# Kernel optimization log

Measured on AMD Instinct MI355X. Metric: run time of the kernel, lower is better.

## Reference

```python
import jax, jax.numpy as jnp
import numpy as np

EPS = 1e-12
N_HEADS = 16


def _ln(x, g, b, eps=EPS):
    m = jnp.mean(x, axis=-1, keepdims=True)
    v = jnp.var(x, axis=-1, keepdims=True)
    return (x - m) * jax.lax.rsqrt(v + eps) * g + b


def setup_inputs() -> dict:
    key = jax.random.key(0)
    ks = jax.random.split(key, 8)
    B, S, D, I = 2, 2048, 1024, 4096
    s = 0.02
    f32 = jnp.float32
    return {
        "x": jax.random.normal(ks[0], (B, S, D), f32),
        "input_mask": jnp.zeros((B, 1, 1, S), f32),  # additive mask, 0 = no masking
        "norm_w": jnp.ones((D,), f32),
        "norm_b": jnp.zeros((D,), f32),
        "attn_qkvw": jax.random.normal(ks[1], (D, 3 * D), f32) * s,
        "attn_qkvb": jnp.zeros((3 * D,), f32),
        "attn_ow": jax.random.normal(ks[2], (D, D), f32) * s,
        "attn_ob": jnp.zeros((D,), f32),
        "attn_nw": jnp.ones((D,), f32),
        "attn_nb": jnp.zeros((D,), f32),
        "inter_w": jax.random.normal(ks[3], (D, I), f32) * s,
        "inter_b": jnp.zeros((I,), f32),
        "inter_w1": jax.random.normal(ks[4], (D, I), f32) * s,
        "output_w": jax.random.normal(ks[5], (I, D), f32) * s,
        "output_b": jnp.zeros((D,), f32),
    }


def reference(x, input_mask, norm_w, norm_b, attn_qkvw, attn_qkvb, attn_ow,
              attn_ob, attn_nw, attn_nb, inter_w, inter_b, inter_w1,
              output_w, output_b):
    B, S, D = x.shape
    hd = D // N_HEADS

    # --- fused qkv_gemm: pre-layernorm + QKV GEMM + bias ---
    ln1 = _ln(x, norm_w, norm_b)
    qkv = ln1 @ attn_qkvw + attn_qkvb            # [B,S,3D]
    q, k, v = jnp.split(qkv, 3, axis=-1)

    def to_heads(t):  # [B,S,D] -> [B,H,S,hd]
        return t.reshape(B, S, N_HEADS, hd).transpose(0, 2, 1, 3)

    q, k, v = to_heads(q), to_heads(k), to_heads(v)

    # --- softmax-context attention (scale_attention=True -> 1/sqrt(head_dim)) ---
    scores = jnp.einsum('bhqd,bhkd->bhqk', q, k) / jnp.sqrt(jnp.float32(hd))
    scores = scores + input_mask                 # additive mask [B,1,1,S]
    probs = jax.nn.softmax(scores, axis=-1)
    ctx = jnp.einsum('bhqk,bhkd->bhqd', probs, v)
    ctx = ctx.transpose(0, 2, 1, 3).reshape(B, S, D)

    attn_out = ctx @ attn_ow                     # vector_matmul (no bias)

    # --- fused mlp_gemm: bias+residual add, layernorm, GEMM+bias+gelu ---
    residual_add = attn_out + attn_ob + x
    ln2 = _ln(residual_add, attn_nw, attn_nb)
    intermediate = jax.nn.gelu(ln2 @ inter_w + inter_b, approximate=False)
    # gated path: vector_matmul(mlp input, inter_w1) * intermediate (per source)
    intermediate = (attn_out @ inter_w1) * intermediate

    # --- output projection + bias_residual ---
    out = intermediate @ output_w + output_b + residual_add
    return out
```

## Files before the change

kernel.cpp:

```cpp
#include <hip/hip_runtime.h>
#include <hip/hip_bf16.h>

#define BATCH 2
#define SEQ   2048
#define DIM   1024
#define IDIM  4096
#define NH    16
#define HD    64
#define TOK   (BATCH * SEQ)

typedef __hip_bfloat16 bf16;

typedef short bf16x8_t __attribute__((ext_vector_type(8)));
typedef float f32x4_t  __attribute__((ext_vector_type(4)));

__device__ __forceinline__ float ldv(const float* p, size_t i) { return p[i]; }
__device__ __forceinline__ float ldv(const bf16*  p, size_t i) { return __bfloat162float(p[i]); }
__device__ __forceinline__ void  stv(float* p, size_t i, float v) { p[i] = v; }
__device__ __forceinline__ void  stv(bf16*  p, size_t i, float v) { p[i] = __float2bfloat16(v); }

__device__ __forceinline__ f32x4_t mfma16(bf16x8_t a, bf16x8_t b, f32x4_t c) {
    return __builtin_amdgcn_mfma_f32_16x16x32_bf16(a, b, c, 0, 0, 0);
}

__device__ __forceinline__ void gload16(const bf16* g, bf16* l) {
    __builtin_amdgcn_global_load_lds(
        (const __attribute__((address_space(1))) void*)g,
        (__attribute__((address_space(3))) void*)l, 16, 0, 0);
}

__device__ __forceinline__ void xcd_map(int &bx, int &by) {
    const int gn  = gridDim.x;
    const int lin = blockIdx.y * gn + blockIdx.x;
    const int cx  = gn >> 3;
    const int xcd = lin & 7;
    const int slot = lin >> 3;
    bx = xcd * cx + slot % cx;
    by = slot / cx;
}

__global__ __launch_bounds__(256) void ln_kernel(const float* __restrict__ in,
                                                 const float* __restrict__ w,
                                                 const float* __restrict__ b,
                                                 bf16* __restrict__ out) {
    const int row = blockIdx.x;
    const int tid = threadIdx.x;
    const float* xr = in + (size_t)row * DIM;

    float v[4], sum = 0.f, sq = 0.f;
#pragma unroll
    for (int i = 0; i < 4; i++) {
        float t = xr[tid + i * 256];
        v[i] = t; sum += t; sq += t * t;
    }
#pragma unroll
    for (int off = 32; off >= 1; off >>= 1) {
        sum += __shfl_xor(sum, off);
        sq  += __shfl_xor(sq,  off);
    }
    __shared__ float s1[4], s2[4];
    int wid = tid >> 6;
    if ((tid & 63) == 0) { s1[wid] = sum; s2[wid] = sq; }
    __syncthreads();
    sum = s1[0] + s1[1] + s1[2] + s1[3];
    sq  = s2[0] + s2[1] + s2[2] + s2[3];

    const float mean = sum * (1.f / DIM);
    const float var  = fmaxf(sq * (1.f / DIM) - mean * mean, 0.f);
    const float rstd = rsqrtf(var + 1e-12f);

    bf16* orow = out + (size_t)row * DIM;
#pragma unroll
    for (int i = 0; i < 4; i++) {
        int idx = tid + i * 256;
        orow[idx] = __float2bfloat16((v[i] - mean) * rstd * w[idx] + b[idx]);
    }
}

__global__ __launch_bounds__(256) void wconv_kernel(const float* __restrict__ W,
                                                    bf16* __restrict__ Wt,
                                                    int K, int N) {
    __shared__ float tile[32][33];
    const int tid = threadIdx.x;
    const int n0 = blockIdx.x * 32;
    const int k0 = blockIdx.y * 32;
    const int c = tid & 31;
    const int r = tid >> 5;
#pragma unroll
    for (int i = 0; i < 4; i++)
        tile[r + i * 8][c] = W[(size_t)(k0 + r + i * 8) * N + n0 + c];
    __syncthreads();
#pragma unroll
    for (int i = 0; i < 4; i++)
        Wt[(size_t)(n0 + r + i * 8) * K + k0 + c] = __float2bfloat16(tile[c][r + i * 8]);
}

#define GBK 32

template<typename TX, int MODE, int TM, int TN>
__global__ __launch_bounds__(256) void mgemm_kernel(const bf16* __restrict__ A,
                                                    const bf16* __restrict__ Bt,
                                                    const float* __restrict__ bias,
                                                    const TX* __restrict__ aux,
                                                    TX* __restrict__ C,
                                                    const float* __restrict__ bias2,
                                                    const float* __restrict__ xin,
                                                    float* __restrict__ C2,
                                                    int M, int N, int K) {
    constexpr int TILE_M = TM * 32;
    constexpr int TILE_N = TN * 32;
    constexpr int LOADS  = TM / 2 + TN / 2;
    __shared__ alignas(16) bf16 As[2][TILE_M][GBK];
    __shared__ alignas(16) bf16 Bs[2][TILE_N][GBK];

    const int tid  = threadIdx.x;
    const int w    = tid >> 6;
    const int lane = tid & 63;
    const int cl   = lane & 15;
    const int qd   = lane >> 4;
    const int wm   = w >> 1;
    const int wn   = w & 1;

    int bx, by;
    xcd_map(bx, by);

    const int row0 = by * TILE_M;
    const int col0 = bx * TILE_N;

    const int lrow = lane >> 2;
    const int lkg  = lane & 3;
    const int sslot = lkg ^ ((lrow >> 1) & 3);
    const int rds   = (cl >> 1) & 3;

    const bf16* gA = A  + (size_t)(row0 + lrow) * K + sslot * 8;
    const bf16* gB = Bt + (size_t)(col0 + lrow) * K + sslot * 8;

    f32x4_t acc[TM][TN];
#pragma unroll
    for (int m = 0; m < TM; m++)
#pragma unroll
        for (int n = 0; n < TN; n++) acc[m][n] = {0.f, 0.f, 0.f, 0.f};

    auto stage = [&](int b, int k0) {
#pragma unroll
        for (int i = 0; i < TM / 2; i++) {
            const int r16 = (w * (TM / 2) + i) * 16;
            gload16(gA + (size_t)r16 * K + k0, &As[b][r16][0]);
        }
#pragma unroll
        for (int j = 0; j < TN / 2; j++) {
            const int r16 = (w * (TN / 2) + j) * 16;
            gload16(gB + (size_t)r16 * K + k0, &Bs[b][r16][0]);
        }
    };

    stage(0, 0);
    stage(1, GBK);
    asm volatile("s_waitcnt vmcnt(%0)" :: "i"(LOADS) : "memory");
    __builtin_amdgcn_s_barrier();

    const int NT = K / GBK;
    for (int t = 0; t < NT; t++) {
        const int cur = t & 1;

        bf16x8_t af[TM], bfr[TN];
#pragma unroll
        for (int m = 0; m < TM; m++)
            af[m] = *(const bf16x8_t*)&As[cur][wm * (TM * 16) + m * 16 + cl][(qd ^ rds) * 8];
#pragma unroll
        for (int n = 0; n < TN; n++)
            bfr[n] = *(const bf16x8_t*)&Bs[cur][wn * (TN * 16) + n * 16 + cl][(qd ^ rds) * 8];
        asm volatile("s_waitcnt lgkmcnt(0)" ::: "memory");
        __builtin_amdgcn_sched_barrier(0);
        __builtin_amdgcn_s_barrier();

        if (t + 2 < NT) stage(cur, (t + 2) * GBK);

        __builtin_amdgcn_s_setprio(1);
#pragma unroll
        for (int m = 0; m < TM; m++)
#pragma unroll
            for (int n = 0; n < TN; n++)
                acc[m][n] = mfma16(af[m], bfr[n], acc[m][n]);
        __builtin_amdgcn_s_setprio(0);

        if (t + 1 < NT) {
            if (t + 2 < NT)
                asm volatile("s_waitcnt vmcnt(%0)" :: "i"(LOADS) : "memory");
            else
                asm volatile("s_waitcnt vmcnt(0)" ::: "memory");
            __builtin_amdgcn_s_barrier();
        }
    }

#pragma unroll
    for (int m = 0; m < TM; m++) {
#pragma unroll
        for (int n = 0; n < TN; n++) {
            const int gc = col0 + wn * (TN * 16) + n * 16 + cl;
            const float bv = (MODE != 4 && bias) ? bias[gc] : 0.f;
#pragma unroll
            for (int r = 0; r < 4; r++) {
                const int gr = row0 + wm * (TM * 16) + m * 16 + qd * 4 + r;
                float c = acc[m][n][r] + bv;
                if (MODE == 3) {
                    c += ldv(aux, (size_t)gr * N + gc);
                }
                stv(C, (size_t)gr * N + gc, c);
                if (MODE == 4) {
                    C2[(size_t)gr * N + gc] = c + bias2[gc] + xin[(size_t)gr * N + gc];
                }
            }
        }
    }
}

__global__ __launch_bounds__(512, 4) void dualgemm_kernel(const bf16* __restrict__ A0,
                                                          const bf16* __restrict__ B0t,
                                                          const bf16* __restrict__ A1,
                                                          const bf16* __restrict__ B1t,
                                                          const float* __restrict__ bias,
                                                          bf16* __restrict__ C,
                                                          int M, int N, int K) {
    __shared__ alignas(16) char pool[66560];

    const int tid  = threadIdx.x;
    const int w    = tid >> 6;
    const int lane = tid & 63;
    const int cl   = lane & 15;
    const int qd   = lane >> 4;
    const int gsel = w >> 2;
    const int g2   = w & 3;
    const int wm   = g2 >> 1;
    const int wn   = g2 & 1;

    int bx, by;
    xcd_map(bx, by);
    const int row0 = by * 128;
    const int col0 = bx * 128;

    const int lrow = lane >> 2;
    const int lkg  = lane & 3;
    const int sslot = lkg ^ ((lrow >> 1) & 3);
    const int rds   = (cl >> 1) & 3;

    const int sarr = w >> 1;
    const bf16* gsrc;
    {
        const bf16* bases[4] = {A0, B0t, A1, B1t};
        const int   r0s[4]   = {row0, col0, row0, col0};
        gsrc = bases[sarr] + (size_t)(r0s[sarr] + lrow) * K + sslot * 8;
    }

    auto sptr = [&](int b, int a) -> bf16* {
        return (bf16*)(pool + b * 32768 + a * 8192);
    };

    f32x4_t acc[4][4];
#pragma unroll
    for (int m = 0; m < 4; m++)
#pragma unroll
        for (int n = 0; n < 4; n++) acc[m][n] = {0.f, 0.f, 0.f, 0.f};

    auto stage = [&](int b, int k0) {
        bf16* dst = sptr(b, sarr);
#pragma unroll
        for (int j = 0; j < 4; j++) {
            const int rg = (w & 1) * 4 + j;
            gload16(gsrc + (size_t)(rg * 16) * K + k0, dst + rg * 16 * GBK);
        }
    };

    stage(0, 0);
    stage(1, GBK);
    asm volatile("s_waitcnt vmcnt(4)" ::: "memory");
    __builtin_amdgcn_s_barrier();

    const int NT = K / GBK;
    for (int t = 0; t < NT; t++) {
        const int cur = t & 1;
        const bf16* Sa = sptr(cur, gsel * 2);
        const bf16* Sb = sptr(cur, gsel * 2 + 1);

        bf16x8_t af[4], bfr[4];
#pragma unroll
        for (int m = 0; m < 4; m++)
            af[m] = *(const bf16x8_t*)&Sa[(wm * 64 + m * 16 + cl) * GBK + (qd ^ rds) * 8];
#pragma unroll
        for (int n = 0; n < 4; n++)
            bfr[n] = *(const bf16x8_t*)&Sb[(wn * 64 + n * 16 + cl) * GBK + (qd ^ rds) * 8];
        asm volatile("s_waitcnt lgkmcnt(0)" ::: "memory");
        __builtin_amdgcn_sched_barrier(0);
        __builtin_amdgcn_s_barrier();

        if (t + 2 < NT) stage(cur, (t + 2) * GBK);

        __builtin_amdgcn_s_setprio(1);
#pragma unroll
        for (int m = 0; m < 4; m++)
#pragma unroll
            for (int n = 0; n < 4; n++)
                acc[m][n] = mfma16(af[m], bfr[n], acc[m][n]);
        __builtin_amdgcn_s_setprio(0);

        if (t + 1 < NT) {
            if (t + 2 < NT)
                asm volatile("s_waitcnt vmcnt(4)" ::: "memory");
            else
                asm volatile("s_waitcnt vmcnt(0)" ::: "memory");
            __builtin_amdgcn_s_barrier();
        }
    }

    float* X = (float*)pool;
    __syncthreads();
    if (gsel == 1) {
#pragma unroll
        for (int m = 0; m < 4; m++)
#pragma unroll
            for (int n = 0; n < 4; n++)
#pragma unroll
                for (int r = 0; r < 4; r++)
                    X[(wm * 64 + m * 16 + qd * 4 + r) * 130 + wn * 64 + n * 16 + cl] =
                        acc[m][n][r];
    }
    __syncthreads();
    if (gsel == 0) {
#pragma unroll
        for (int m = 0; m < 4; m++) {
#pragma unroll
            for (int n = 0; n < 4; n++) {
                const int lc = wn * 64 + n * 16 + cl;
                const int gc = col0 + lc;
                const float bv = bias[gc];
#pragma unroll
                for (int r = 0; r < 4; r++) {
                    const int lr = wm * 64 + m * 16 + qd * 4 + r;
                    float g = acc[m][n][r] + bv;
                    g = 0.5f * g * (1.f + erff(g * 0.70710678118654752f));
                    C[(size_t)(row0 + lr) * N + gc] = __float2bfloat16(g * X[lr * 130 + lc]);
                }
            }
        }
    }
}

__global__ __launch_bounds__(256) void vtrans_kernel(const bf16* __restrict__ qkv,
                                                     bf16* __restrict__ vt) {
    __shared__ bf16 t[64][72];
    const int tid = threadIdx.x;
    const int s0  = blockIdx.x * 64;
    const int bh  = blockIdx.y;
    const int bb  = bh >> 4;
    const int h   = bh & 15;
    const bf16* src = qkv + (size_t)bb * SEQ * (3 * DIM) + 2 * DIM + h * HD;
    const int r  = tid >> 3;
    const int cc = tid & 7;
#pragma unroll
    for (int i = 0; i < 2; i++)
        *(bf16x8_t*)&t[r + i * 32][cc * 8] =
            *(const bf16x8_t*)(src + (size_t)(s0 + r + i * 32) * (3 * DIM) + cc * 8);
    __syncthreads();
    bf16* dst = vt + (size_t)bh * HD * SEQ + s0;
#pragma unroll
    for (int i = 0; i < 2; i++) {
        const int d = r + i * 32;
        bf16x8_t v;
#pragma unroll
        for (int j = 0; j < 8; j++)
            ((short*)&v)[j] = *(const short*)&t[cc * 8 + j][d];
        *(bf16x8_t*)(dst + (size_t)d * SEQ + cc * 8) = v;
    }
}

#define KCH 64
#define NCH (SEQ / KCH)

__device__ __forceinline__ unsigned pk2(float lo, float hi) {
    unsigned a = (unsigned)__bfloat16_as_ushort(__float2bfloat16(lo));
    unsigned b = (unsigned)__bfloat16_as_ushort(__float2bfloat16(hi));
    return a | (b << 16);
}

union PAU { bf16x8_t v; unsigned u[4]; };

__global__ __launch_bounds__(256, 2) void attn_mfma_kernel(const bf16* __restrict__ qkv,
                                                           const bf16* __restrict__ vt,
                                                           const float* __restrict__ mask,
                                                           bf16* __restrict__ ctx) {
    __shared__ alignas(16) bf16 Kl[2][KCH][64];
    __shared__ alignas(16) bf16 Vl[2][KCH][64];

    const int tid  = threadIdx.x;
    const int w    = tid >> 6;
    const int lane = tid & 63;
    const int cl   = lane & 15;
    const int qd   = lane >> 4;
    const int c7   = cl & 7;

    const int qtile = blockIdx.x;
    const int bh    = blockIdx.y;
    const int bb    = bh >> 4;
    const int h     = bh & 15;

    const bf16*  base = qkv + (size_t)bb * SEQ * (3 * DIM) + h * HD;
    const bf16*  gK   = base + DIM;
    const bf16*  gV   = vt + (size_t)bh * HD * SEQ;
    const float* mrow = mask + (size_t)bb * SEQ;

    bf16x8_t aq[2][2];
#pragma unroll
    for (int qt = 0; qt < 2; qt++) {
        const bf16* qrow = base + (size_t)(qtile * 128 + w * 32 + qt * 16 + cl) * (3 * DIM);
        aq[qt][0] = *(const bf16x8_t*)(qrow + qd * 8);
        aq[qt][1] = *(const bf16x8_t*)(qrow + 32 + qd * 8);
    }

    const bf16x8_t onesv = {0x3F80, 0x3F80, 0x3F80, 0x3F80,
                            0x3F80, 0x3F80, 0x3F80, 0x3F80};

    const int sr  = lane >> 3;
    const int scw = (lane & 7) ^ sr;

#pragma unroll
    for (int i = 0; i < 2; i++) {
        const int row = i * 32 + w * 8 + sr;
        gload16(gK + (size_t)row * (3 * DIM) + scw * 8, &Kl[0][i * 32 + w * 8][0]);
        gload16(gV + (size_t)row * SEQ + scw * 8, &Vl[0][i * 32 + w * 8][0]);
    }
    f32x4_t mkx[4];
#pragma unroll
    for (int ks = 0; ks < 4; ks++)
        mkx[ks] = *(const f32x4_t*)&mrow[ks * 16 + qd * 4];

    f32x4_t O[2][4];
#pragma unroll
    for (int qt = 0; qt < 2; qt++)
#pragma unroll
        for (int ns = 0; ns < 4; ns++) O[qt][ns] = {0.f, 0.f, 0.f, 0.f};
    f32x4_t li[2] = {{0.f,0.f,0.f,0.f},{0.f,0.f,0.f,0.f}};

    for (int c = 0; c < NCH; c++) {
        __syncthreads();
        const bf16 (*Kb)[64] = Kl[c & 1];
        const bf16 (*Vb)[64] = Vl[c & 1];

        f32x4_t mk[4];
#pragma unroll
        for (int ks = 0; ks < 4; ks++) mk[ks] = mkx[ks];

        if (c + 1 < NCH) {
            bf16 (*Kn)[64] = Kl[(c + 1) & 1];
            bf16 (*Vn)[64] = Vl[(c + 1) & 1];
            const int k0n = (c + 1) * KCH;
#pragma unroll
            for (int i = 0; i < 2; i++) {
                const int row = i * 32 + w * 8 + sr;
                gload16(gK + (size_t)(k0n + row) * (3 * DIM) + scw * 8, &Kn[i * 32 + w * 8][0]);
                gload16(gV + (size_t)row * SEQ + k0n + scw * 8, &Vn[i * 32 + w * 8][0]);
            }
#pragma unroll
            for (int ks = 0; ks < 4; ks++)
                mkx[ks] = *(const f32x4_t*)&mrow[k0n + ks * 16 + qd * 4];
        }

        bf16x8_t kf[4][2];
#pragma unroll
        for (int ks = 0; ks < 4; ks++) {
            kf[ks][0] = *(const bf16x8_t*)&Kb[ks * 16 + cl][(qd ^ c7) << 3];
            kf[ks][1] = *(const bf16x8_t*)&Kb[ks * 16 + cl][((4 + qd) ^ c7) << 3];
        }

        PAU pa[2][2];
#pragma unroll
        for (int qt = 0; qt < 2; qt++) {
            unsigned Dv[4][2];
#pragma unroll
            for (int ks = 0; ks < 4; ks++) {
                f32x4_t s = {0.f, 0.f, 0.f, 0.f};
                s = mfma16(kf[ks][0], aq[qt][0], s);
                s = mfma16(kf[ks][1], aq[qt][1], s);
                const float e0 = __expf(s[0] * 0.125f + mk[ks][0]);
                const float e1 = __expf(s[1] * 0.125f + mk[ks][1]);
                const float e2 = __expf(s[2] * 0.125f + mk[ks][2]);
                const float e3 = __expf(s[3] * 0.125f + mk[ks][3]);
                Dv[ks][0] = pk2(e0, e1);
                Dv[ks][1] = pk2(e2, e3);
            }
#pragma unroll
            for (int rp = 0; rp < 2; rp++) {
                auto z0 = __builtin_amdgcn_permlane32_swap(Dv[0][rp], Dv[1][rp], false, false);
                auto w0 = __builtin_amdgcn_permlane16_swap(z0[0], z0[1], false, false);
                pa[qt][0].u[rp]     = w0[0];
                pa[qt][0].u[rp + 2] = w0[1];
                auto z1 = __builtin_amdgcn_permlane32_swap(Dv[2][rp], Dv[3][rp], false, false);
                auto w1 = __builtin_amdgcn_permlane16_swap(z1[0], z1[1], false, false);
                pa[qt][1].u[rp]     = w1[0];
                pa[qt][1].u[rp + 2] = w1[1];
            }
            f32x4_t ls = {0.f, 0.f, 0.f, 0.f};
            ls = mfma16(pa[qt][0].v, onesv, ls);
            ls = mfma16(pa[qt][1].v, onesv, ls);
            li[qt] += ls;
        }

#pragma unroll
        for (int ns = 0; ns < 4; ns++) {
            bf16x8_t v0 = *(const bf16x8_t*)&Vb[ns * 16 + cl][(qd ^ c7) << 3];
            bf16x8_t v1 = *(const bf16x8_t*)&Vb[ns * 16 + cl][((4 + qd) ^ c7) << 3];
#pragma unroll
            for (int qt = 0; qt < 2; qt++) {
                O[qt][ns] = mfma16(pa[qt][0].v, v0, O[qt][ns]);
                O[qt][ns] = mfma16(pa[qt][1].v, v1, O[qt][ns]);
            }
        }
    }

#pragma unroll
    for (int qt = 0; qt < 2; qt++) {
#pragma unroll
        for (int r = 0; r < 4; r++) {
            const int row = qtile * 128 + w * 32 + qt * 16 + qd * 4 + r;
            bf16* orow = ctx + (size_t)(bb * SEQ + row) * DIM + h * HD;
            const float inv = 1.f / li[qt][r];
#pragma unroll
            for (int ns = 0; ns < 4; ns++)
                orow[ns * 16 + cl] = __float2bfloat16(O[qt][ns][r] * inv);
        }
    }
}

extern "C" void kernel_launch(void* const* d_in, const int* in_sizes, int n_in,
                              void* d_out, int out_size, void* d_ws, size_t ws_size,
                              hipStream_t stream) {
    const float* x        = (const float*)d_in[0];
    const float* mask     = (const float*)d_in[1];
    const float* norm_w   = (const float*)d_in[2];
    const float* norm_b   = (const float*)d_in[3];
    const float* qkvw     = (const float*)d_in[4];
    const float* qkvb     = (const float*)d_in[5];
    const float* attn_ow  = (const float*)d_in[6];
    const float* attn_ob  = (const float*)d_in[7];
    const float* attn_nw  = (const float*)d_in[8];
    const float* attn_nb  = (const float*)d_in[9];
    const float* inter_w  = (const float*)d_in[10];
    const float* inter_b  = (const float*)d_in[11];
    const float* inter_w1 = (const float*)d_in[12];
    const float* output_w = (const float*)d_in[13];
    const float* output_b = (const float*)d_in[14];

    float* out = (float*)d_out;
    bf16*  ws  = (bf16*)d_ws;

    const size_t M1 = 1024 * 1024;
    bf16* ln_s      = ws;
    bf16* qkv       = ws + 4 * M1;
    bf16* inter     = ws + 4 * M1;
    bf16* qkvw_t    = ws + 16 * M1;
    bf16* attn_owt  = ws + 19 * M1;
    bf16* vt        = ws + 20 * M1;
    bf16* attn_out  = ws + 20 * M1;
    bf16* inter_wt  = ws + 24 * M1;
    bf16* inter_w1t = ws + 28 * M1;
    bf16* output_wt = ws + 32 * M1;
    float* resid    = out;

    dim3 blk(256);

    wconv_kernel<<<dim3(3072 / 32, 1024 / 32), blk, 0, stream>>>(qkvw,     qkvw_t,    1024, 3072);
    wconv_kernel<<<dim3(1024 / 32, 1024 / 32), blk, 0, stream>>>(attn_ow,  attn_owt,  1024, 1024);
    wconv_kernel<<<dim3(4096 / 32, 1024 / 32), blk, 0, stream>>>(inter_w,  inter_wt,  1024, 4096);
    wconv_kernel<<<dim3(4096 / 32, 1024 / 32), blk, 0, stream>>>(inter_w1, inter_w1t, 1024, 4096);
    wconv_kernel<<<dim3(1024 / 32, 4096 / 32), blk, 0, stream>>>(output_w, output_wt, 4096, 1024);

    ln_kernel<<<TOK, blk, 0, stream>>>(x, norm_w, norm_b, ln_s);

    mgemm_kernel<bf16, 0, 4, 4><<<dim3(3072 / 128, TOK / 128), blk, 0, stream>>>(
        ln_s, qkvw_t, qkvb, (const bf16*)nullptr, qkv,
        nullptr, nullptr, nullptr, TOK, 3 * DIM, DIM);

    vtrans_kernel<<<dim3(SEQ / 64, BATCH * NH), blk, 0, stream>>>(qkv, vt);

    attn_mfma_kernel<<<dim3(SEQ / 128, BATCH * NH), blk, 0, stream>>>(qkv, vt, mask, ln_s);

    mgemm_kernel<bf16, 4, 4, 2><<<dim3(DIM / 64, TOK / 128), blk, 0, stream>>>(
        ln_s, attn_owt, (const float*)nullptr, (const bf16*)nullptr, attn_out,
        attn_ob, x, resid, TOK, DIM, DIM);

    ln_kernel<<<TOK, blk, 0, stream>>>(resid, attn_nw, attn_nb, ln_s);

    dualgemm_kernel<<<dim3(IDIM / 128, TOK / 128), dim3(512), 0, stream>>>(
        ln_s, inter_wt, attn_out, inter_w1t, inter_b, inter, TOK, IDIM, DIM);

    mgemm_kernel<float, 3, 4, 2><<<dim3(DIM / 64, TOK / 128), blk, 0, stream>>>(
        inter, output_wt, output_b, resid, out,
        nullptr, nullptr, nullptr, TOK, DIM, IDIM);
}
```

Measured before the change: 449.9 us.

## Run mgemm with eight waves per block and split warp tiling

Moves the generic MFMA GEMM from 4 to 8 waves per block, keeping the same block tile. The warp grid changes to 2x4 or 4x2 depending on TN, so each wave holds fewer accumulator fragments, and the global-to-LDS staging is redistributed so each wave issues one A load and possibly one B load per stage. Per-wave vmcnt waits are adjusted to match. The aim is more latency hiding and higher occupancy. The cost is more barrier participants and fewer MFMAs per LDS fragment load, since each wave reuses less data.

```diff
diff --git a/kernel.cpp b/kernel.cpp
--- a/kernel.cpp
+++ b/kernel.cpp
@@ -98,18 +98,22 @@
 #define GBK 32
 
 template<typename TX, int MODE, int TM, int TN>
-__global__ __launch_bounds__(256) void mgemm_kernel(const bf16* __restrict__ A,
-                                                    const bf16* __restrict__ Bt,
-                                                    const float* __restrict__ bias,
-                                                    const TX* __restrict__ aux,
-                                                    TX* __restrict__ C,
-                                                    const float* __restrict__ bias2,
-                                                    const float* __restrict__ xin,
-                                                    float* __restrict__ C2,
-                                                    int M, int N, int K) {
+__global__ __launch_bounds__(512, 4) void mgemm_kernel(const bf16* __restrict__ A,
+                                                       const bf16* __restrict__ Bt,
+                                                       const float* __restrict__ bias,
+                                                       const TX* __restrict__ aux,
+                                                       TX* __restrict__ C,
+                                                       const float* __restrict__ bias2,
+                                                       const float* __restrict__ xin,
+                                                       float* __restrict__ C2,
+                                                       int M, int N, int K) {
     constexpr int TILE_M = TM * 32;
     constexpr int TILE_N = TN * 32;
-    constexpr int LOADS  = TM / 2 + TN / 2;
+    constexpr int WN = (TN >= 4) ? 4 : 2;
+    constexpr int WM = 8 / WN;
+    constexpr int MF = (TM * 2) / WM;
+    constexpr int NF = (TN * 2) / WN;
+    constexpr int RG = 2 * (TM + TN);
     __shared__ alignas(16) bf16 As[2][TILE_M][GBK];
     __shared__ alignas(16) bf16 Bs[2][TILE_N][GBK];
 
@@ -118,8 +122,8 @@
     const int lane = tid & 63;
     const int cl   = lane & 15;
     const int qd   = lane >> 4;
-    const int wm   = w >> 1;
-    const int wn   = w & 1;
+    const int wm   = w / WN;
+    const int wn   = w % WN;
 
     int bx, by;
     xcd_map(bx, by);
@@ -135,41 +139,45 @@
     const bf16* gA = A  + (size_t)(row0 + lrow) * K + sslot * 8;
     const bf16* gB = Bt + (size_t)(col0 + lrow) * K + sslot * 8;
 
-    f32x4_t acc[TM][TN];
-#pragma unroll
-    for (int m = 0; m < TM; m++)
-#pragma unroll
-        for (int n = 0; n < TN; n++) acc[m][n] = {0.f, 0.f, 0.f, 0.f};
+    f32x4_t acc[MF][NF];
+#pragma unroll
+    for (int m = 0; m < MF; m++)
+#pragma unroll
+        for (int n = 0; n < NF; n++) acc[m][n] = {0.f, 0.f, 0.f, 0.f};
 
     auto stage = [&](int b, int k0) {
-#pragma unroll
-        for (int i = 0; i < TM / 2; i++) {
-            const int r16 = (w * (TM / 2) + i) * 16;
-            gload16(gA + (size_t)r16 * K + k0, &As[b][r16][0]);
-        }
-#pragma unroll
-        for (int j = 0; j < TN / 2; j++) {
-            const int r16 = (w * (TN / 2) + j) * 16;
-            gload16(gB + (size_t)r16 * K + k0, &Bs[b][r16][0]);
-        }
+        {
+            const int rg = w;
+            gload16(gA + (size_t)(rg * 16) * K + k0, &As[b][rg * 16][0]);
+        }
+        if (w + 8 < RG) {
+            const int rgb = w + 8 - 2 * TM;
+            gload16(gB + (size_t)(rgb * 16) * K + k0, &Bs[b][rgb * 16][0]);
+        }
+    };
+    auto wait_stage = [&]() {
+        if (RG == 16 || w < RG - 8)
+            asm volatile("s_waitcnt vmcnt(2)" ::: "memory");
+        else
+            asm volatile("s_waitcnt vmcnt(1)" ::: "memory");
     };
 
     stage(0, 0);
     stage(1, GBK);
-    asm volatile("s_waitcnt vmcnt(%0)" :: "i"(LOADS) : "memory");
+    wait_stage();
     __builtin_amdgcn_s_barrier();
 
     const int NT = K / GBK;
     for (int t = 0; t < NT; t++) {
         const int cur = t & 1;
 
-        bf16x8_t af[TM], bfr[TN];
-#pragma unroll
-        for (int m = 0; m < TM; m++)
-            af[m] = *(const bf16x8_t*)&As[cur][wm * (TM * 16) + m * 16 + cl][(qd ^ rds) * 8];
-#pragma unroll
-        for (int n = 0; n < TN; n++)
-            bfr[n] = *(const bf16x8_t*)&Bs[cur][wn * (TN * 16) + n * 16 + cl][(qd ^ rds) * 8];
+        bf16x8_t af[MF], bfr[NF];
+#pragma unroll
+        for (int m = 0; m < MF; m++)
+            af[m] = *(const bf16x8_t*)&As[cur][wm * (MF * 16) + m * 16 + cl][(qd ^ rds) * 8];
+#pragma unroll
+        for (int n = 0; n < NF; n++)
+            bfr[n] = *(const bf16x8_t*)&Bs[cur][wn * (NF * 16) + n * 16 + cl][(qd ^ rds) * 8];
         asm volatile("s_waitcnt lgkmcnt(0)" ::: "memory");
         __builtin_amdgcn_sched_barrier(0);
         __builtin_amdgcn_s_barrier();
@@ -178,15 +186,15 @@
 
         __builtin_amdgcn_s_setprio(1);
 #pragma unroll
-        for (int m = 0; m < TM; m++)
-#pragma unroll
-            for (int n = 0; n < TN; n++)
+        for (int m = 0; m < MF; m++)
+#pragma unroll
+            for (int n = 0; n < NF; n++)
                 acc[m][n] = mfma16(af[m], bfr[n], acc[m][n]);
         __builtin_amdgcn_s_setprio(0);
 
         if (t + 1 < NT) {
             if (t + 2 < NT)
-                asm volatile("s_waitcnt vmcnt(%0)" :: "i"(LOADS) : "memory");
+                wait_stage();
             else
                 asm volatile("s_waitcnt vmcnt(0)" ::: "memory");
             __builtin_amdgcn_s_barrier();
@@ -194,14 +202,14 @@
     }
 
 #pragma unroll
-    for (int m = 0; m < TM; m++) {
-#pragma unroll
-        for (int n = 0; n < TN; n++) {
-            const int gc = col0 + wn * (TN * 16) + n * 16 + cl;
+    for (int m = 0; m < MF; m++) {
+#pragma unroll
+        for (int n = 0; n < NF; n++) {
+            const int gc = col0 + wn * (NF * 16) + n * 16 + cl;
             const float bv = (MODE != 4 && bias) ? bias[gc] : 0.f;
 #pragma unroll
             for (int r = 0; r < 4; r++) {
-                const int gr = row0 + wm * (TM * 16) + m * 16 + qd * 4 + r;
+                const int gr = row0 + wm * (MF * 16) + m * 16 + qd * 4 + r;
                 float c = acc[m][n][r] + bv;
                 if (MODE == 3) {
                     c += ldv(aux, (size_t)gr * N + gc);
@@ -566,6 +574,7 @@
     float* resid    = out;
 
     dim3 blk(256);
+    dim3 blk512(512);
 
     wconv_kernel<<<dim3(3072 / 32, 1024 / 32), blk, 0, stream>>>(qkvw,     qkvw_t,    1024, 3072);
     wconv_kernel<<<dim3(1024 / 32, 1024 / 32), blk, 0, stream>>>(attn_ow,  attn_owt,  1024, 1024);
@@ -575,7 +584,7 @@
 
     ln_kernel<<<TOK, blk, 0, stream>>>(x, norm_w, norm_b, ln_s);
 
-    mgemm_kernel<bf16, 0, 4, 4><<<dim3(3072 / 128, TOK / 128), blk, 0, stream>>>(
+    mgemm_kernel<bf16, 0, 4, 4><<<dim3(3072 / 128, TOK / 128), blk512, 0, stream>>>(
         ln_s, qkvw_t, qkvb, (const bf16*)nullptr, qkv,
         nullptr, nullptr, nullptr, TOK, 3 * DIM, DIM);
 
@@ -583,16 +592,16 @@
 
     attn_mfma_kernel<<<dim3(SEQ / 128, BATCH * NH), blk, 0, stream>>>(qkv, vt, mask, ln_s);
 
-    mgemm_kernel<bf16, 4, 4, 2><<<dim3(DIM / 64, TOK / 128), blk, 0, stream>>>(
+    mgemm_kernel<bf16, 4, 4, 2><<<dim3(DIM / 64, TOK / 128), blk512, 0, stream>>>(
         ln_s, attn_owt, (const float*)nullptr, (const bf16*)nullptr, attn_out,
         attn_ob, x, resid, TOK, DIM, DIM);
 
     ln_kernel<<<TOK, blk, 0, stream>>>(resid, attn_nw, attn_nb, ln_s);
 
-    dualgemm_kernel<<<dim3(IDIM / 128, TOK / 128), dim3(512), 0, stream>>>(
+    dualgemm_kernel<<<dim3(IDIM / 128, TOK / 128), blk512, 0, stream>>>(
         ln_s, inter_wt, attn_out, inter_w1t, inter_b, inter, TOK, IDIM, DIM);
 
-    mgemm_kernel<float, 3, 4, 2><<<dim3(DIM / 64, TOK / 128), blk, 0, stream>>>(
+    mgemm_kernel<float, 3, 4, 2><<<dim3(DIM / 64, TOK / 128), blk512, 0, stream>>>(
         inter, output_wt, output_b, resid, out,
         nullptr, nullptr, nullptr, TOK, DIM, IDIM);
 }
```

New measurement: 453.1 us. Within noise of the previous version (+0.7%).
